# Kernel tuning notes

Hardware: AMD Instinct MI355X
Metric: run time of the kernel (lower is better)

Reference implementation:

```python
import jax, jax.numpy as jnp
import numpy as np
from jax import lax


def _lstm_layer(c, h, xs, Wi, Wh, b):
    """Scan flax OptimizedLSTMCell math over time. xs: (B, T, F)."""
    def step(carry, xt):
        c, h = carry
        z = xt @ Wi + h @ Wh + b  # (B, 4H)
        i, f, g, o = jnp.split(z, 4, axis=-1)  # flax gate order: i, f, g, o
        c_new = jax.nn.sigmoid(f) * c + jax.nn.sigmoid(i) * jnp.tanh(g)
        h_new = jax.nn.sigmoid(o) * jnp.tanh(c_new)
        return (c_new, h_new), h_new
    (c_f, h_f), ys = lax.scan(step, (c, h), jnp.swapaxes(xs, 0, 1))  # scan over T
    return (c_f, h_f), jnp.swapaxes(ys, 0, 1)  # back to (B, T, H)


def setup_inputs() -> dict:
    key = jax.random.key(0)
    ks = jax.random.split(key, 16)
    B, T, F, H, W, A = 128, 256, 128, 256, 512, 8
    s = 0.02  # small init scale to avoid saturating tanh/sigmoid
    return {
        "x": jax.random.normal(ks[0], (B, T, F), jnp.float32),
        "c0": jnp.zeros((B, H), jnp.float32),
        "h0": jnp.zeros((B, H), jnp.float32),
        "c1": jnp.zeros((B, H), jnp.float32),
        "h1": jnp.zeros((B, H), jnp.float32),
        "Wi0": jax.random.normal(ks[1], (F, 4 * H), jnp.float32) * s,
        "Wh0": jax.random.normal(ks[2], (H, 4 * H), jnp.float32) * s,
        "b0": jnp.zeros((4 * H,), jnp.float32),
        "Wi1": jax.random.normal(ks[3], (H, 4 * H), jnp.float32) * s,
        "Wh1": jax.random.normal(ks[4], (H, 4 * H), jnp.float32) * s,
        "b1": jnp.zeros((4 * H,), jnp.float32),
        "Wv0": jax.random.normal(ks[5], (T * H, W), jnp.float32) * s,
        "bv0": jnp.zeros((W,), jnp.float32),
        "Wv1": jax.random.normal(ks[6], (W, W), jnp.float32) * s,
        "bv1": jnp.zeros((W,), jnp.float32),
        "Wv2": jax.random.normal(ks[7], (W, 1), jnp.float32) * s,
        "bv2": jnp.zeros((1,), jnp.float32),
        "Wm0": jax.random.normal(ks[8], (T * H, W), jnp.float32) * s,
        "bm0": jnp.zeros((W,), jnp.float32),
        "Wm1": jax.random.normal(ks[9], (W, W), jnp.float32) * s,
        "bm1": jnp.zeros((W,), jnp.float32),
        "Wm2": jax.random.normal(ks[10], (W, A), jnp.float32) * s,
        "bm2": jnp.zeros((A,), jnp.float32),
        "log_std": jnp.zeros((A,), jnp.float32),
    }


def reference(x, c0, h0, c1, h1, Wi0, Wh0, b0, Wi1, Wh1, b1,
              Wv0, bv0, Wv1, bv1, Wv2, bv2,
              Wm0, bm0, Wm1, bm1, Wm2, bm2, log_std):
    # stacked recurrent layers
    (c0n, h0n), x = _lstm_layer(c0, h0, x, Wi0, Wh0, b0)
    (c1n, h1n), x = _lstm_layer(c1, h1, x, Wi1, Wh1, b1)
    flat = x.reshape(x.shape[0], -1)  # (B, T*H)
    # value head (n_layers=2 hidden + output)
    value = jnp.tanh(flat @ Wv0 + bv0)
    value = jnp.tanh(value @ Wv1 + bv1)
    value = value @ Wv2 + bv2  # (B, 1)
    # mean head
    mean = jnp.tanh(flat @ Wm0 + bm0)
    mean = jnp.tanh(mean @ Wm1 + bm1)
    mean = mean @ Wm2 + bm2  # (B, A)
    return (mean, log_std, value, ((c0n, h0n), (c1n, h1n)))
```

## Files before the change

kernel.cpp:

```cpp
#include <hip/hip_runtime.h>


typedef __attribute__((ext_vector_type(8))) short  frag8;
typedef __attribute__((ext_vector_type(4))) float  f32x4;
typedef unsigned short u16;
typedef unsigned int   u32;

#define WS_FLAGS 0
#define WS_XT    16384
#define WS_W0B   (WS_XT + 128*256*128*2)
#define WS_W1B   (WS_W0B + 262144)
#define WS_YS0   (WS_W1B + 524288)
#define WS_YS1   (WS_YS0 + 16777216)
#define WS_H0M   (WS_YS1 + 16777216)
#define WS_V1M   (WS_H0M + 262144)
#define WS_P     WS_XT

__device__ __forceinline__ u16 f2b(float f) {
  u32 u = __builtin_bit_cast(u32, f);
  u32 r = (u + 0x7fffu + ((u >> 16) & 1u)) >> 16;
  return (u16)r;
}
__device__ __forceinline__ float b2f(u16 b) {
  return __builtin_bit_cast(float, (u32)b << 16);
}
__device__ __forceinline__ float sigm(float x) { return 1.0f / (1.0f + __expf(-x)); }
__device__ __forceinline__ float tanh_(float x) {
  x = fminf(fmaxf(x, -15.0f), 15.0f);
  float e = __expf(2.0f * x);
  return (e - 1.0f) / (e + 1.0f);
}

__device__ __forceinline__ frag8 coh16(const u16* p) {
  frag8 r;
  asm volatile("global_load_dwordx4 %0, %1, off sc0 sc1" : "=v"(r) : "v"(p) : "memory");
  return r;
}
__device__ __forceinline__ frag8 ld16c(const u16* p) {
  frag8 r;
  asm volatile("global_load_dwordx4 %0, %1, off" : "=v"(r) : "v"(p) : "memory");
  return r;
}
__device__ __forceinline__ void coh_st32(u16* p, u32 v) {
  asm volatile("global_store_dword %0, %1, off sc0 sc1" :: "v"(p), "v"(v) : "memory");
}
__device__ __forceinline__ u32 coh_ld32(const u32* p) {
  u32 r;
  asm volatile("global_load_dword %0, %1, off sc0 sc1\n\t"
               "s_waitcnt vmcnt(0)" : "=v"(r) : "v"(p) : "memory");
  return r;
}
__device__ __forceinline__ void waitall() {
  asm volatile("s_waitcnt vmcnt(0)" ::: "memory");
  __builtin_amdgcn_sched_barrier(0);
}

__device__ __forceinline__ void postcnt(u32* p) {
  asm volatile("s_waitcnt vmcnt(0)" ::: "memory");
  __syncthreads();
  if (threadIdx.x == 0)
    __hip_atomic_fetch_add(p, 1u, __ATOMIC_RELAXED, __HIP_MEMORY_SCOPE_AGENT);
}
__device__ __forceinline__ void pollwait(const u32* p, u32 tgt, bool act) {
  if (threadIdx.x < 64) {
    while (true) {
      u32 v = act ? coh_ld32(p) : tgt;
      if (!__any(v < tgt)) break;
      __builtin_amdgcn_s_sleep(1);
    }
  }
  __syncthreads();
}

__global__ void convert_x_kernel(const float* __restrict__ x, u16* __restrict__ xT) {
  int g = blockIdx.x * 256 + threadIdx.x;
  int f4 = g & 31, rem = g >> 5;
  int t = rem >> 7, b = rem & 127;
  const float4 v = *reinterpret_cast<const float4*>(x + ((size_t)(b * 256 + t)) * 128 + f4 * 4);
  ushort4 ov;
  ov.x = f2b(v.x); ov.y = f2b(v.y); ov.z = f2b(v.z); ov.w = f2b(v.w);
  *reinterpret_cast<ushort4*>(xT + (size_t)rem * 128 + f4 * 4) = ov;
}

__global__ void wxb_kernel(const float* __restrict__ Wi0, const float* __restrict__ Wi1,
                           u16* __restrict__ w0b, u16* __restrict__ w1b) {
  int g = blockIdx.x * 256 + threadIdx.x;
  const float* W; u16* dst; int NKX, fi;
  if (g < 16384) { W = Wi0; dst = w0b; NKX = 4; fi = g; }
  else           { W = Wi1; dst = w1b; NKX = 8; fi = g - 16384; }
  int l = fi & 63; int rest = fi >> 6;
  int kt = rest % NKX; rest /= NKX;
  int tile = rest & 3; int blk = rest >> 2;
  int gcol = tile * 256 + blk * 16 + (l & 15);
  int k0 = kt * 32 + (l >> 4) * 8;
#pragma unroll
  for (int j = 0; j < 8; ++j)
    dst[(size_t)fi * 8 + j] = f2b(W[(size_t)(k0 + j) * 1024 + gcol]);
}

template <int NKX, int LAYER>
__device__ __forceinline__ void lstm_body(
    const u16* __restrict__ xsrc, int xstride, const u16* __restrict__ wxb,
    const float* __restrict__ Wh, const float* __restrict__ bias,
    const float* __restrict__ cin, const float* __restrict__ hin,
    u16* __restrict__ ys, float* __restrict__ cOut, float* __restrict__ hOut,
    u32* __restrict__ ctr0, u32* __restrict__ ctr1, int blk) {
  const int tid = threadIdx.x, wv = tid >> 6, l = tid & 63;
  const int cl = l & 15, lk8 = (l >> 4) * 8;
  const int hdb = blk * 16, hd = hdb + cl;
  u32* ctrSelf = (LAYER == 0) ? ctr0 : ctr1;

  frag8 wh[4][8];
#pragma unroll
  for (int g = 0; g < 4; ++g) {
    int gcol = g * 256 + hdb + cl;
#pragma unroll
    for (int kt = 0; kt < 8; ++kt) {
      frag8 f;
#pragma unroll
      for (int j = 0; j < 8; ++j)
        f[j] = (short)f2b(Wh[(size_t)(kt * 32 + lk8 + j) * 1024 + gcol]);
      wh[g][kt] = f;
    }
  }
  float bi[4];
#pragma unroll
  for (int g = 0; g < 4; ++g) bi[g] = bias[g * 256 + hdb + cl];
  float cst[2][4];
#pragma unroll
  for (int rt = 0; rt < 2; ++rt)
#pragma unroll
    for (int r = 0; r < 4; ++r)
      cst[rt][r] = cin[(wv * 32 + rt * 16 + (l >> 4) * 4 + r) * 256 + hd];

#pragma unroll 1
  for (int t = 0; t < 256; ++t) {
    frag8 xa[2][NKX], ha[2][8];

    if (LAYER == 0) {
      const u16* xb = xsrc + (size_t)t * 128 * xstride;
#pragma unroll
      for (int rt = 0; rt < 2; ++rt) {
        int arow = wv * 32 + rt * 16 + cl;
#pragma unroll
        for (int kt = 0; kt < NKX; ++kt)
          xa[rt][kt] = ld16c(xb + (size_t)arow * xstride + kt * 32 + lk8);
      }
      if (t > 0)
        pollwait(ctr0 + (t - 1) * 4, 16u, l == 0);
    } else {
      const u32* p = (l == 1 && t > 0) ? (ctr1 + (t - 1) * 4) : (ctr0 + t * 4);
      bool act = (l == 0) || (l == 1 && t > 0);
      pollwait(p, 16u, act);
      const u16* xb = xsrc + (size_t)t * 128 * xstride;
#pragma unroll
      for (int rt = 0; rt < 2; ++rt) {
        int arow = wv * 32 + rt * 16 + cl;
#pragma unroll
        for (int kt = 0; kt < NKX; ++kt)
          xa[rt][kt] = coh16(xb + (size_t)arow * xstride + kt * 32 + lk8);
      }
    }

    if (t == 0) {
#pragma unroll
      for (int rt = 0; rt < 2; ++rt) {
        int arow = wv * 32 + rt * 16 + cl;
        const float* hp = hin + arow * 256;
#pragma unroll
        for (int kt = 0; kt < 8; ++kt) {
          const float* p = hp + kt * 32 + lk8;
          float4 q0 = *(const float4*)p, q1 = *(const float4*)(p + 4);
          frag8 f;
          f[0] = (short)f2b(q0.x); f[1] = (short)f2b(q0.y);
          f[2] = (short)f2b(q0.z); f[3] = (short)f2b(q0.w);
          f[4] = (short)f2b(q1.x); f[5] = (short)f2b(q1.y);
          f[6] = (short)f2b(q1.z); f[7] = (short)f2b(q1.w);
          ha[rt][kt] = f;
        }
      }
    } else {
      const u16* hb = ys + ((size_t)(t - 1) << 15);
#pragma unroll
      for (int rt = 0; rt < 2; ++rt) {
        int arow = wv * 32 + rt * 16 + cl;
#pragma unroll
        for (int kt = 0; kt < 8; ++kt)
          ha[rt][kt] = coh16(hb + arow * 256 + kt * 32 + lk8);
      }
    }

    f32x4 acc[4][2];
#pragma unroll
    for (int g = 0; g < 4; ++g)
#pragma unroll
      for (int rt = 0; rt < 2; ++rt)
        acc[g][rt] = f32x4{bi[g], bi[g], bi[g], bi[g]};

    if (LAYER == 0) {
#pragma unroll
      for (int kt = 0; kt < NKX; ++kt)
#pragma unroll
        for (int g = 0; g < 4; ++g) {
          frag8 wf = *(const frag8*)(wxb + ((((size_t)blk * 4 + g) * NKX + kt) * 64 + l) * 8);
          acc[g][0] = __builtin_amdgcn_mfma_f32_16x16x32_bf16(xa[0][kt], wf, acc[g][0], 0, 0, 0);
          acc[g][1] = __builtin_amdgcn_mfma_f32_16x16x32_bf16(xa[1][kt], wf, acc[g][1], 0, 0, 0);
        }
      waitall();
    } else {
      waitall();
#pragma unroll
      for (int kt = 0; kt < NKX; ++kt)
#pragma unroll
        for (int g = 0; g < 4; ++g) {
          frag8 wf = *(const frag8*)(wxb + ((((size_t)blk * 4 + g) * NKX + kt) * 64 + l) * 8);
          acc[g][0] = __builtin_amdgcn_mfma_f32_16x16x32_bf16(xa[0][kt], wf, acc[g][0], 0, 0, 0);
          acc[g][1] = __builtin_amdgcn_mfma_f32_16x16x32_bf16(xa[1][kt], wf, acc[g][1], 0, 0, 0);
        }
    }
#pragma unroll
    for (int kt = 0; kt < 8; ++kt)
#pragma unroll
      for (int g = 0; g < 4; ++g) {
        acc[g][0] = __builtin_amdgcn_mfma_f32_16x16x32_bf16(ha[0][kt], wh[g][kt], acc[g][0], 0, 0, 0);
        acc[g][1] = __builtin_amdgcn_mfma_f32_16x16x32_bf16(ha[1][kt], wh[g][kt], acc[g][1], 0, 0, 0);
      }

    u16* yd = ys + ((size_t)t << 15);
#pragma unroll
    for (int rt = 0; rt < 2; ++rt)
#pragma unroll
      for (int r = 0; r < 4; ++r) {
        int row = wv * 32 + rt * 16 + (l >> 4) * 4 + r;
        float zi = acc[0][rt][r], zf = acc[1][rt][r];
        float zg = acc[2][rt][r], zo = acc[3][rt][r];
        float cn = sigm(zf) * cst[rt][r] + sigm(zi) * tanh_(zg);
        float hn = sigm(zo) * tanh_(cn);
        cst[rt][r] = cn;
        u32 hb16 = (u32)f2b(hn);
        u32 pr = (u32)__shfl_xor((int)hb16, 1);
        if ((cl & 1) == 0)
          coh_st32(yd + row * 256 + hd, hb16 | (pr << 16));
        if (t == 255) {
          cOut[row * 256 + hd] = cn;
          hOut[row * 256 + hd] = hn;
        }
      }
    postcnt(ctrSelf + t * 4);
  }
}

__launch_bounds__(256, 1)
__global__ void lstm_fused(const u16* __restrict__ xT,
                           const u16* __restrict__ w0b, const u16* __restrict__ w1b,
                           const float* __restrict__ Wh0, const float* __restrict__ b0,
                           const float* __restrict__ c0, const float* __restrict__ h0,
                           const float* __restrict__ Wh1, const float* __restrict__ b1,
                           const float* __restrict__ c1, const float* __restrict__ h1,
                           u16* __restrict__ ys0, u16* __restrict__ ys1,
                           float* __restrict__ out, u32* __restrict__ flags) {
  const int gid = blockIdx.x;
  u32* ctr0 = flags;
  u32* ctr1 = flags + 1024;
  if (gid < 16)
    lstm_body<4, 0>(xT, 128, w0b, Wh0, b0, c0, h0, ys0,
                    out + 1160, out + 33928, ctr0, ctr1, gid);
  else
    lstm_body<8, 1>(ys0, 256, w1b, Wh1, b1, c1, h1, ys1,
                    out + 66696, out + 99464, ctr0, ctr1, gid - 16);
}

__launch_bounds__(256, 2)
__global__ void head_gemm_kernel(const u16* __restrict__ flatT,
                                 const float* __restrict__ Wv0,
                                 const float* __restrict__ Wm0,
                                 float* __restrict__ P) {
  const int bx = blockIdx.x;
  const int nb = bx >> 5, kb = bx & 31;
  const float* W = (nb >> 3) ? Wm0 : Wv0;
  const int ncb = (nb & 7) * 64;
  const int tid = threadIdx.x;
  const int wv = tid >> 6, l = tid & 63;
  const int lrow = l & 15, lk = (l >> 4) * 8;
  f32x4 acc[2][4] = {};
  const int kbase = kb * 2048;
#pragma unroll 2
  for (int ks = 0; ks < 64; ++ks) {
    int k0 = kbase + ks * 32;
    int t = k0 >> 8, h = k0 & 255;
    frag8 a[2];
#pragma unroll
    for (int mi = 0; mi < 2; ++mi) {
      int row = (2 * wv + mi) * 16 + lrow;
      a[mi] = *reinterpret_cast<const frag8*>(flatT + ((size_t)t * 128 + row) * 256 + h + lk);
    }
#pragma unroll
    for (int nt = 0; nt < 4; ++nt) {
      int col = ncb + nt * 16 + lrow;
      const float* wp = W + (size_t)(k0 + lk) * 512 + col;
      frag8 bfrag;
#pragma unroll
      for (int j = 0; j < 8; ++j) bfrag[j] = (short)f2b(wp[(size_t)j * 512]);
      acc[0][nt] = __builtin_amdgcn_mfma_f32_16x16x32_bf16(a[0], bfrag, acc[0][nt], 0, 0, 0);
      acc[1][nt] = __builtin_amdgcn_mfma_f32_16x16x32_bf16(a[1], bfrag, acc[1][nt], 0, 0, 0);
    }
  }
  float* Pb = P + (size_t)bx * 8192;
#pragma unroll
  for (int mi = 0; mi < 2; ++mi)
#pragma unroll
    for (int nt = 0; nt < 4; ++nt)
#pragma unroll
      for (int r = 0; r < 4; ++r) {
        int row = (2 * wv + mi) * 16 + (l >> 4) * 4 + r;
        int nl = nt * 16 + lrow;
        Pb[row * 64 + nl] = acc[mi][nt][r];
      }
}

__global__ void head_reduce_kernel(const float* __restrict__ P,
                                   const float* __restrict__ bv0,
                                   const float* __restrict__ bm0,
                                   u16* __restrict__ H0) {
  int o = blockIdx.x * 256 + threadIdx.x;
  int row = o >> 10, gcol = o & 1023;
  int nb = gcol >> 6, nl = gcol & 63;
  float s = 0.f;
#pragma unroll
  for (int kb = 0; kb < 32; ++kb)
    s += P[(size_t)(nb * 32 + kb) * 8192 + row * 64 + nl];
  s += (gcol < 512) ? bv0[gcol] : bm0[gcol - 512];
  H0[row * 1024 + gcol] = f2b(tanh_(s));
}

__launch_bounds__(256, 2)
__global__ void head_mid_kernel(const u16* __restrict__ H0,
                                const float* __restrict__ Wv1,
                                const float* __restrict__ Wm1,
                                const float* __restrict__ bv1,
                                const float* __restrict__ bm1,
                                u16* __restrict__ V1M) {
  const int nb = blockIdx.x;
  const int head = nb >> 3;
  const int ncb = (nb & 7) * 64;
  const float* W = head ? Wm1 : Wv1;
  const float* bsrc = head ? bm1 : bv1;
  const int tid = threadIdx.x, wv = tid >> 6, l = tid & 63;
  const int lrow = l & 15, lk = (l >> 4) * 8;
  const int aoff = head * 512;
  f32x4 acc[2][4] = {};
#pragma unroll 2
  for (int ks = 0; ks < 16; ++ks) {
    int k0 = ks * 32;
    frag8 a[2];
#pragma unroll
    for (int mi = 0; mi < 2; ++mi) {
      int row = (2 * wv + mi) * 16 + lrow;
      a[mi] = *reinterpret_cast<const frag8*>(H0 + row * 1024 + aoff + k0 + lk);
    }
#pragma unroll
    for (int nt = 0; nt < 4; ++nt) {
      int col = ncb + nt * 16 + lrow;
      const float* wp = W + (size_t)(k0 + lk) * 512 + col;
      frag8 bfrag;
#pragma unroll
      for (int j = 0; j < 8; ++j) bfrag[j] = (short)f2b(wp[(size_t)j * 512]);
      acc[0][nt] = __builtin_amdgcn_mfma_f32_16x16x32_bf16(a[0], bfrag, acc[0][nt], 0, 0, 0);
      acc[1][nt] = __builtin_amdgcn_mfma_f32_16x16x32_bf16(a[1], bfrag, acc[1][nt], 0, 0, 0);
    }
  }
#pragma unroll
  for (int mi = 0; mi < 2; ++mi)
#pragma unroll
    for (int nt = 0; nt < 4; ++nt)
#pragma unroll
      for (int r = 0; r < 4; ++r) {
        int row = (2 * wv + mi) * 16 + (l >> 4) * 4 + r;
        int cl = ncb + nt * 16 + lrow;
        float z = acc[mi][nt][r] + bsrc[cl];
        V1M[row * 1024 + head * 512 + cl] = f2b(tanh_(z));
      }
}

__global__ void head_final_kernel(const u16* __restrict__ V1M,
                                  const float* __restrict__ Wv2,
                                  const float* __restrict__ bv2,
                                  const float* __restrict__ Wm2,
                                  const float* __restrict__ bm2,
                                  const float* __restrict__ log_std,
                                  float* __restrict__ out) {
  int tid = threadIdx.x;
  {
    int row = tid >> 3, a = tid & 7;
    float s = 0.f;
    for (int k = 0; k < 512; ++k)
      s += b2f(V1M[row * 1024 + 512 + k]) * Wm2[k * 8 + a];
    out[row * 8 + a] = s + bm2[a];
  }
  if (tid < 128) {
    float s = 0.f;
    for (int k = 0; k < 512; ++k)
      s += b2f(V1M[tid * 1024 + k]) * Wv2[k];
    out[1032 + tid] = s + bv2[0];
  }
  if (tid < 8) out[1024 + tid] = log_std[tid];
}

extern "C" void kernel_launch(void* const* d_in, const int* in_sizes, int n_in,
                              void* d_out, int out_size, void* d_ws, size_t ws_size,
                              hipStream_t stream) {
  const float* x    = (const float*)d_in[0];
  const float* c0   = (const float*)d_in[1];
  const float* h0   = (const float*)d_in[2];
  const float* c1   = (const float*)d_in[3];
  const float* h1   = (const float*)d_in[4];
  const float* Wi0  = (const float*)d_in[5];
  const float* Wh0  = (const float*)d_in[6];
  const float* b0   = (const float*)d_in[7];
  const float* Wi1  = (const float*)d_in[8];
  const float* Wh1  = (const float*)d_in[9];
  const float* b1   = (const float*)d_in[10];
  const float* Wv0  = (const float*)d_in[11];
  const float* bv0  = (const float*)d_in[12];
  const float* Wv1  = (const float*)d_in[13];
  const float* bv1  = (const float*)d_in[14];
  const float* Wv2  = (const float*)d_in[15];
  const float* bv2  = (const float*)d_in[16];
  const float* Wm0  = (const float*)d_in[17];
  const float* bm0  = (const float*)d_in[18];
  const float* Wm1  = (const float*)d_in[19];
  const float* bm1  = (const float*)d_in[20];
  const float* Wm2  = (const float*)d_in[21];
  const float* bm2  = (const float*)d_in[22];
  const float* lstd = (const float*)d_in[23];
  float* out = (float*)d_out;
  char* ws = (char*)d_ws;

  u32* flags = (u32*)(ws + WS_FLAGS);
  u16* xT    = (u16*)(ws + WS_XT);
  u16* w0b   = (u16*)(ws + WS_W0B);
  u16* w1b   = (u16*)(ws + WS_W1B);
  u16* ys0   = (u16*)(ws + WS_YS0);
  u16* ys1   = (u16*)(ws + WS_YS1);
  float* P   = (float*)(ws + WS_P);
  u16* H0M   = (u16*)(ws + WS_H0M);
  u16* V1M   = (u16*)(ws + WS_V1M);

  hipMemsetAsync(ws + WS_FLAGS, 0, 16384, stream);
  convert_x_kernel<<<4096, 256, 0, stream>>>(x, xT);
  wxb_kernel<<<192, 256, 0, stream>>>(Wi0, Wi1, w0b, w1b);
  lstm_fused<<<32, 256, 0, stream>>>(xT, w0b, w1b, Wh0, b0, c0, h0,
                                     Wh1, b1, c1, h1, ys0, ys1, out, flags);
  head_gemm_kernel<<<512, 256, 0, stream>>>(ys1, Wv0, Wm0, P);
  head_reduce_kernel<<<512, 256, 0, stream>>>(P, bv0, bm0, H0M);
  head_mid_kernel<<<16, 256, 0, stream>>>(H0M, Wv1, Wm1, bv1, bm1, V1M);
  head_final_kernel<<<1, 1024, 0, stream>>>(V1M, Wv2, bv2, Wm2, bm2, lstd, out);
}
```

Baseline: 3.015 ms.

## Replace counter-flag barriers with poisoned-data polling between LSTM blocks

Removes the per-step atomic counters and poll-waits used to synchronise the 32 persistent LSTM blocks. Instead, the ys0/ys1 buffers are pre-filled with an all-ones sentinel, and each block spins on coherent loads of its h and x inputs until no sentinel words remain. This cuts a __syncthreads, an atomic and a separate flag round-trip from each timestep. The risks are that the sentinel could collide with a real bf16 pair (0xFFFF is a NaN pattern), that a 32 MB poison fill is added to every call, and that the loop gives up after a bounded number of tries.

New measurement: 4.017 ms. 33.2% more time.

```diff
diff --git a/kernel.cpp b/kernel.cpp
--- a/kernel.cpp
+++ b/kernel.cpp
@@ -3,10 +3,10 @@
 
 typedef __attribute__((ext_vector_type(8))) short  frag8;
 typedef __attribute__((ext_vector_type(4))) float  f32x4;
+typedef __attribute__((ext_vector_type(4))) unsigned int u32x4;
 typedef unsigned short u16;
 typedef unsigned int   u32;
 
-#define WS_FLAGS 0
 #define WS_XT    16384
 #define WS_W0B   (WS_XT + 128*256*128*2)
 #define WS_W1B   (WS_W0B + 262144)
@@ -44,32 +44,24 @@
 __device__ __forceinline__ void coh_st32(u16* p, u32 v) {
   asm volatile("global_store_dword %0, %1, off sc0 sc1" :: "v"(p), "v"(v) : "memory");
 }
-__device__ __forceinline__ u32 coh_ld32(const u32* p) {
-  u32 r;
-  asm volatile("global_load_dword %0, %1, off sc0 sc1\n\t"
-               "s_waitcnt vmcnt(0)" : "=v"(r) : "v"(p) : "memory");
-  return r;
-}
 __device__ __forceinline__ void waitall() {
   asm volatile("s_waitcnt vmcnt(0)" ::: "memory");
   __builtin_amdgcn_sched_barrier(0);
 }
-
-__device__ __forceinline__ void postcnt(u32* p) {
-  asm volatile("s_waitcnt vmcnt(0)" ::: "memory");
-  __syncthreads();
-  if (threadIdx.x == 0)
-    __hip_atomic_fetch_add(p, 1u, __ATOMIC_RELAXED, __HIP_MEMORY_SCOPE_AGENT);
-}
-__device__ __forceinline__ void pollwait(const u32* p, u32 tgt, bool act) {
-  if (threadIdx.x < 64) {
-    while (true) {
-      u32 v = act ? coh_ld32(p) : tgt;
-      if (!__any(v < tgt)) break;
-      __builtin_amdgcn_s_sleep(1);
-    }
-  }
-  __syncthreads();
+__device__ __forceinline__ u32 pz(frag8 f) {
+  u32x4 w = __builtin_bit_cast(u32x4, f);
+  u32 b = 0;
+  b |= (w[0] == 0xFFFFFFFFu) ? 1u : 0u;
+  b |= (w[1] == 0xFFFFFFFFu) ? 1u : 0u;
+  b |= (w[2] == 0xFFFFFFFFu) ? 1u : 0u;
+  b |= (w[3] == 0xFFFFFFFFu) ? 1u : 0u;
+  return b;
+}
+
+__global__ void poison_kernel(u32* __restrict__ p) {
+  size_t g = (size_t)blockIdx.x * 256 + threadIdx.x;
+  u32x4 v = {0xFFFFFFFFu, 0xFFFFFFFFu, 0xFFFFFFFFu, 0xFFFFFFFFu};
+  *reinterpret_cast<u32x4*>(p + g * 4) = v;
 }
 
 __global__ void convert_x_kernel(const float* __restrict__ x, u16* __restrict__ xT) {
@@ -104,11 +96,11 @@
     const float* __restrict__ Wh, const float* __restrict__ bias,
     const float* __restrict__ cin, const float* __restrict__ hin,
     u16* __restrict__ ys, float* __restrict__ cOut, float* __restrict__ hOut,
-    u32* __restrict__ ctr0, u32* __restrict__ ctr1, int blk) {
+    int blk) {
   const int tid = threadIdx.x, wv = tid >> 6, l = tid & 63;
   const int cl = l & 15, lk8 = (l >> 4) * 8;
   const int hdb = blk * 16, hd = hdb + cl;
-  u32* ctrSelf = (LAYER == 0) ? ctr0 : ctr1;
+  const int arow0 = wv * 32 + cl;
 
   frag8 wh[4][8];
 #pragma unroll
@@ -136,37 +128,20 @@
 #pragma unroll 1
   for (int t = 0; t < 256; ++t) {
     frag8 xa[2][NKX], ha[2][8];
+    const u16* xb = xsrc + (size_t)t * 128 * xstride;
 
     if (LAYER == 0) {
-      const u16* xb = xsrc + (size_t)t * 128 * xstride;
+#pragma unroll
+      for (int rt = 0; rt < 2; ++rt)
+#pragma unroll
+        for (int kt = 0; kt < NKX; ++kt)
+          xa[rt][kt] = ld16c(xb + (size_t)(arow0 + rt * 16) * xstride + kt * 32 + lk8);
+    }
+
+    if (t == 0) {
 #pragma unroll
       for (int rt = 0; rt < 2; ++rt) {
-        int arow = wv * 32 + rt * 16 + cl;
-#pragma unroll
-        for (int kt = 0; kt < NKX; ++kt)
-          xa[rt][kt] = ld16c(xb + (size_t)arow * xstride + kt * 32 + lk8);
-      }
-      if (t > 0)
-        pollwait(ctr0 + (t - 1) * 4, 16u, l == 0);
-    } else {
-      const u32* p = (l == 1 && t > 0) ? (ctr1 + (t - 1) * 4) : (ctr0 + t * 4);
-      bool act = (l == 0) || (l == 1 && t > 0);
-      pollwait(p, 16u, act);
-      const u16* xb = xsrc + (size_t)t * 128 * xstride;
-#pragma unroll
-      for (int rt = 0; rt < 2; ++rt) {
-        int arow = wv * 32 + rt * 16 + cl;
-#pragma unroll
-        for (int kt = 0; kt < NKX; ++kt)
-          xa[rt][kt] = coh16(xb + (size_t)arow * xstride + kt * 32 + lk8);
-      }
-    }
-
-    if (t == 0) {
-#pragma unroll
-      for (int rt = 0; rt < 2; ++rt) {
-        int arow = wv * 32 + rt * 16 + cl;
-        const float* hp = hin + arow * 256;
+        const float* hp = hin + (arow0 + rt * 16) * 256;
 #pragma unroll
         for (int kt = 0; kt < 8; ++kt) {
           const float* p = hp + kt * 32 + lk8;
@@ -179,14 +154,56 @@
           ha[rt][kt] = f;
         }
       }
+      if (LAYER == 1) {
+        int tries = 0;
+        while (true) {
+#pragma unroll
+          for (int rt = 0; rt < 2; ++rt)
+#pragma unroll
+            for (int kt = 0; kt < NKX; ++kt)
+              xa[rt][kt] = coh16(xb + (size_t)(arow0 + rt * 16) * xstride + kt * 32 + lk8);
+          waitall();
+          u32 bad = 0;
+#pragma unroll
+          for (int rt = 0; rt < 2; ++rt)
+#pragma unroll
+            for (int kt = 0; kt < NKX; ++kt) bad |= pz(xa[rt][kt]);
+          if (!__any(bad != 0u)) break;
+          if (++tries > 65536) break;
+        }
+      } else {
+        waitall();
+      }
     } else {
       const u16* hb = ys + ((size_t)(t - 1) << 15);
-#pragma unroll
-      for (int rt = 0; rt < 2; ++rt) {
-        int arow = wv * 32 + rt * 16 + cl;
-#pragma unroll
-        for (int kt = 0; kt < 8; ++kt)
-          ha[rt][kt] = coh16(hb + arow * 256 + kt * 32 + lk8);
+      int tries = 0;
+      while (true) {
+        if (LAYER == 1) {
+#pragma unroll
+          for (int rt = 0; rt < 2; ++rt)
+#pragma unroll
+            for (int kt = 0; kt < NKX; ++kt)
+              xa[rt][kt] = coh16(xb + (size_t)(arow0 + rt * 16) * xstride + kt * 32 + lk8);
+        }
+#pragma unroll
+        for (int rt = 0; rt < 2; ++rt)
+#pragma unroll
+          for (int kt = 0; kt < 8; ++kt)
+            ha[rt][kt] = coh16(hb + (arow0 + rt * 16) * 256 + kt * 32 + lk8);
+        waitall();
+        u32 bad = 0;
+        if (LAYER == 1) {
+#pragma unroll
+          for (int rt = 0; rt < 2; ++rt)
+#pragma unroll
+            for (int kt = 0; kt < NKX; ++kt) bad |= pz(xa[rt][kt]);
+        }
+#pragma unroll
+        for (int rt = 0; rt < 2; ++rt)
+#pragma unroll
+          for (int kt = 0; kt < 8; ++kt) bad |= pz(ha[rt][kt]);
+        if (!__any(bad != 0u)) break;
+        if (++tries > 65536) break;
       }
     }
 
@@ -197,27 +214,14 @@
       for (int rt = 0; rt < 2; ++rt)
         acc[g][rt] = f32x4{bi[g], bi[g], bi[g], bi[g]};
 
-    if (LAYER == 0) {
-#pragma unroll
-      for (int kt = 0; kt < NKX; ++kt)
-#pragma unroll
-        for (int g = 0; g < 4; ++g) {
-          frag8 wf = *(const frag8*)(wxb + ((((size_t)blk * 4 + g) * NKX + kt) * 64 + l) * 8);
-          acc[g][0] = __builtin_amdgcn_mfma_f32_16x16x32_bf16(xa[0][kt], wf, acc[g][0], 0, 0, 0);
-          acc[g][1] = __builtin_amdgcn_mfma_f32_16x16x32_bf16(xa[1][kt], wf, acc[g][1], 0, 0, 0);
-        }
-      waitall();
-    } else {
-      waitall();
-#pragma unroll
-      for (int kt = 0; kt < NKX; ++kt)
-#pragma unroll
-        for (int g = 0; g < 4; ++g) {
-          frag8 wf = *(const frag8*)(wxb + ((((size_t)blk * 4 + g) * NKX + kt) * 64 + l) * 8);
-          acc[g][0] = __builtin_amdgcn_mfma_f32_16x16x32_bf16(xa[0][kt], wf, acc[g][0], 0, 0, 0);
-          acc[g][1] = __builtin_amdgcn_mfma_f32_16x16x32_bf16(xa[1][kt], wf, acc[g][1], 0, 0, 0);
-        }
-    }
+#pragma unroll
+    for (int kt = 0; kt < NKX; ++kt)
+#pragma unroll
+      for (int g = 0; g < 4; ++g) {
+        frag8 wf = *(const frag8*)(wxb + ((((size_t)blk * 4 + g) * NKX + kt) * 64 + l) * 8);
+        acc[g][0] = __builtin_amdgcn_mfma_f32_16x16x32_bf16(xa[0][kt], wf, acc[g][0], 0, 0, 0);
+        acc[g][1] = __builtin_amdgcn_mfma_f32_16x16x32_bf16(xa[1][kt], wf, acc[g][1], 0, 0, 0);
+      }
 #pragma unroll
     for (int kt = 0; kt < 8; ++kt)
 #pragma unroll
@@ -246,7 +250,6 @@
           hOut[row * 256 + hd] = hn;
         }
       }
-    postcnt(ctrSelf + t * 4);
   }
 }
 
@@ -258,16 +261,14 @@
                            const float* __restrict__ Wh1, const float* __restrict__ b1,
                            const float* __restrict__ c1, const float* __restrict__ h1,
                            u16* __restrict__ ys0, u16* __restrict__ ys1,
-                           float* __restrict__ out, u32* __restrict__ flags) {
+                           float* __restrict__ out) {
   const int gid = blockIdx.x;
-  u32* ctr0 = flags;
-  u32* ctr1 = flags + 1024;
   if (gid < 16)
     lstm_body<4, 0>(xT, 128, w0b, Wh0, b0, c0, h0, ys0,
-                    out + 1160, out + 33928, ctr0, ctr1, gid);
+                    out + 1160, out + 33928, gid);
   else
     lstm_body<8, 1>(ys0, 256, w1b, Wh1, b1, c1, h1, ys1,
-                    out + 66696, out + 99464, ctr0, ctr1, gid - 16);
+                    out + 66696, out + 99464, gid - 16);
 }
 
 __launch_bounds__(256, 2)
@@ -436,7 +437,6 @@
   float* out = (float*)d_out;
   char* ws = (char*)d_ws;
 
-  u32* flags = (u32*)(ws + WS_FLAGS);
   u16* xT    = (u16*)(ws + WS_XT);
   u16* w0b   = (u16*)(ws + WS_W0B);
   u16* w1b   = (u16*)(ws + WS_W1B);
@@ -446,11 +446,11 @@
   u16* H0M   = (u16*)(ws + WS_H0M);
   u16* V1M   = (u16*)(ws + WS_V1M);
 
-  hipMemsetAsync(ws + WS_FLAGS, 0, 16384, stream);
+  poison_kernel<<<8192, 256, 0, stream>>>((u32*)(ws + WS_YS0));
   convert_x_kernel<<<4096, 256, 0, stream>>>(x, xT);
   wxb_kernel<<<192, 256, 0, stream>>>(Wi0, Wi1, w0b, w1b);
   lstm_fused<<<32, 256, 0, stream>>>(xT, w0b, w1b, Wh0, b0, c0, h0,
-                                     Wh1, b1, c1, h1, ys0, ys1, out, flags);
+                                     Wh1, b1, c1, h1, ys0, ys1, out);
   head_gemm_kernel<<<512, 256, 0, stream>>>(ys1, Wv0, Wm0, P);
   head_reduce_kernel<<<512, 256, 0, stream>>>(P, bv0, bm0, H0M);
   head_mid_kernel<<<16, 256, 0, stream>>>(H0M, Wv1, Wm1, bv1, bm1, V1M);
```
